# Optimization experiments

Measured on AMD Instinct MI355X. Metric: run time of the kernel, lower is better.

## Reference

```python
import jax, jax.numpy as jnp
import numpy as np

B, S, HID, NH = 2, 2048, 1024, 16
HD = HID // NH  # head dim = 64


def setup_inputs() -> dict:
    key = jax.random.key(0)
    ks = jax.random.split(key, 8)
    sc = 0.02
    return {
        "hidden_states": jax.random.normal(ks[0], (B, S, HID), jnp.float32),
        "hidden_states2": jax.random.normal(ks[1], (B, S, HID), jnp.float32),
        "Wq": jax.random.normal(ks[2], (HID, HID), jnp.float32) * sc,
        "bq": jnp.zeros((HID,), jnp.float32),
        "Wk": jax.random.normal(ks[3], (HID, HID), jnp.float32) * sc,
        "bk": jnp.zeros((HID,), jnp.float32),
        "Wv": jax.random.normal(ks[4], (HID, HID), jnp.float32) * sc,
        "bv": jnp.zeros((HID,), jnp.float32),
    }


def _split_heads(x):
    # [B, S, HID] -> [B, NH, S, HD]
    b, s, _ = x.shape
    return x.reshape(b, s, NH, HD).transpose(0, 2, 1, 3)


def reference(hidden_states, hidden_states2, Wq, bq, Wk, bk, Wv, bv):
    # Linear layers use torch convention: y = x @ W.T + b
    q = _split_heads(hidden_states @ Wq.T + bq)    # [B,NH,Sq,HD]
    k = _split_heads(hidden_states2 @ Wk.T + bk)   # [B,NH,Sk,HD]
    v = _split_heads(hidden_states2 @ Wv.T + bv)   # [B,NH,Sk,HD]
    scores = jnp.einsum("bhqd,bhkd->bhqk", q, k) / jnp.sqrt(jnp.float32(HD))
    probs = jax.nn.softmax(scores, axis=-1)        # dropout prob = 0 (eval)
    ctx = jnp.einsum("bhqk,bhkd->bhqd", probs, v)  # [B,NH,Sq,HD]
    ctx = ctx.transpose(0, 2, 1, 3).reshape(hidden_states.shape[0], hidden_states.shape[1], HID)
    return ctx
```

## Files before the change

### kernel.cpp

```cpp
#include <hip/hip_runtime.h>
#include <hip/hip_bf16.h>
#include <stdint.h>

#define B_   2
#define S_   2048
#define HID_ 1024
#define NH_  16
#define HD_  64

typedef __attribute__((ext_vector_type(4))) float f32x4;
typedef __attribute__((ext_vector_type(8))) short bf16x8;

__device__ inline unsigned short f2bf(float x) {
    __hip_bfloat16 h = __float2bfloat16(x);
    return reinterpret_cast<unsigned short&>(h);
}

__device__ inline void gload_lds16(const void* g, void* l) {
    __builtin_amdgcn_global_load_lds(
        (const __attribute__((address_space(1))) void*)g,
        (__attribute__((address_space(3))) void*)l, 16, 0, 0);
}

__device__ inline float fast_exp2(float x) {
    float r;
    asm("v_exp_f32 %0, %1" : "=v"(r) : "v"(x));
    return r;
}

__global__ __launch_bounds__(256) void cvt_all(
    const float* __restrict__ X1, const float* __restrict__ X2,
    const float* __restrict__ Wq, const float* __restrict__ Wk, const float* __restrict__ Wv,
    unsigned short* __restrict__ X1b, unsigned short* __restrict__ X2b,
    unsigned short* __restrict__ Wqb, unsigned short* __restrict__ Wkb,
    unsigned short* __restrict__ Wvb)
{
    const int id = blockIdx.x;
    const float* src;
    unsigned short* dst;
    int base;
    if (id < 2048)      { src = X1; dst = X1b; base = id; }
    else if (id < 4096) { src = X2; dst = X2b; base = id - 2048; }
    else if (id < 4608) { src = Wq; dst = Wqb; base = id - 4096; }
    else if (id < 5120) { src = Wk; dst = Wkb; base = id - 4608; }
    else                { src = Wv; dst = Wvb; base = id - 5120; }
    const size_t off = (size_t)base * 2048 + (size_t)threadIdx.x * 8;
    float4 a = *(const float4*)&src[off];
    float4 b = *(const float4*)&src[off + 4];
    unsigned short o[8] = {f2bf(a.x), f2bf(a.y), f2bf(a.z), f2bf(a.w),
                           f2bf(b.x), f2bf(b.y), f2bf(b.z), f2bf(b.w)};
    *(uint4*)&dst[off] = *(uint4*)o;
}

__global__ __launch_bounds__(256, 3) void qkv_gemm(
    const unsigned short* __restrict__ X1b, const unsigned short* __restrict__ X2b,
    const unsigned short* __restrict__ Wqb, const unsigned short* __restrict__ Wkb,
    const unsigned short* __restrict__ Wvb,
    const float* __restrict__ bq, const float* __restrict__ bk, const float* __restrict__ bv,
    unsigned short* __restrict__ Qo, unsigned short* __restrict__ Ko, unsigned short* __restrict__ Vo)
{
    const int z = blockIdx.z;
    const unsigned short* X = (z == 0) ? X1b : X2b;
    const unsigned short* W = (z == 0) ? Wqb : (z == 1 ? Wkb : Wvb);
    const float* bias = (z == 0) ? bq : (z == 1 ? bk : bv);
    unsigned short* out = (z == 0) ? Qo : (z == 1 ? Ko : Vo);

    __shared__ __align__(16) unsigned short SM[128 * 132];
    unsigned short* As = SM;
    unsigned short* Bs = SM + 128 * 64;

    const int m0 = blockIdx.x * 128;
    const int n0 = blockIdx.y * 128;
    const int t = threadIdx.x;
    const int lane = t & 63;
    const int w = t >> 6;
    const int lo = lane & 15, hi = lane >> 4;
    const int wm = w >> 1, wn = w & 1;

    const int srow = lane >> 3;
    const int scol = ((lane & 7) ^ srow) * 8;

    f32x4 acc[4][4];
    const f32x4 fzero = {0.f, 0.f, 0.f, 0.f};
    #pragma unroll
    for (int i = 0; i < 4; ++i)
        #pragma unroll
        for (int j = 0; j < 4; ++j) acc[i][j] = fzero;

    for (int kt = 0; kt < 16; ++kt) {
        __syncthreads();
        #pragma unroll
        for (int i = 0; i < 4; ++i) {
            const int r = w * 32 + i * 8 + srow;
            gload_lds16(&X[(size_t)(m0 + r) * HID_ + kt * 64 + scol],
                        &As[w * 2048 + i * 512]);
            gload_lds16(&W[(size_t)(n0 + r) * HID_ + kt * 64 + scol],
                        &Bs[w * 2048 + i * 512]);
        }
        __syncthreads();

        #pragma unroll
        for (int s = 0; s < 2; ++s) {
            const int rcol = ((s * 4 + hi) ^ (lo & 7)) * 8;
            bf16x8 a[4], b[4];
            #pragma unroll
            for (int i = 0; i < 4; ++i) {
                a[i] = *(const bf16x8*)&As[(wm * 64 + i * 16 + lo) * 64 + rcol];
                b[i] = *(const bf16x8*)&Bs[(wn * 64 + i * 16 + lo) * 64 + rcol];
            }
            #pragma unroll
            for (int i = 0; i < 4; ++i)
                #pragma unroll
                for (int j = 0; j < 4; ++j)
                    acc[i][j] = __builtin_amdgcn_mfma_f32_16x16x32_bf16(a[i], b[j], acc[i][j], 0, 0, 0);
        }
    }

    if (z != 2) {
        const float sc = (z == 0) ? 0.18033688011112042f : 1.0f;
        #pragma unroll
        for (int i = 0; i < 4; ++i) {
            #pragma unroll
            for (int j = 0; j < 4; ++j) {
                int col = n0 + wn * 64 + j * 16 + lo;
                float bb = bias[col];
                #pragma unroll
                for (int r = 0; r < 4; ++r) {
                    int row = m0 + wm * 64 + i * 16 + hi * 4 + r;
                    out[(size_t)row * HID_ + col] = f2bf((acc[i][j][r] + bb) * sc);
                }
            }
        }
    } else {
        __syncthreads();
        unsigned short* Ts = SM;
        #pragma unroll
        for (int i = 0; i < 4; ++i) {
            #pragma unroll
            for (int j = 0; j < 4; ++j) {
                int nl = wn * 64 + j * 16 + lo;
                float bb = bias[n0 + nl];
                int ml = wm * 64 + i * 16 + hi * 4;
                ushort4 pk;
                pk.x = f2bf(acc[i][j][0] + bb);
                pk.y = f2bf(acc[i][j][1] + bb);
                pk.z = f2bf(acc[i][j][2] + bb);
                pk.w = f2bf(acc[i][j][3] + bb);
                *(ushort4*)&Ts[nl * 132 + ml] = pk;
            }
        }
        __syncthreads();
        const int nn = t >> 1;
        const int mh = (t & 1) * 64;
        const int bI = m0 >> 11;
        const int sb = (m0 & 2047) + mh;
        size_t obase = (size_t)bI * ((size_t)HID_ * S_) + (size_t)(n0 + nn) * S_ + sb;
        #pragma unroll
        for (int kk = 0; kk < 8; ++kk)
            *(uint4*)&out[obase + kk * 8] = *(const uint4*)&Ts[nn * 132 + mh + kk * 8];
    }
}

__global__ __launch_bounds__(256, 2) void attn_fwd(
    const unsigned short* __restrict__ Q, const unsigned short* __restrict__ K,
    const unsigned short* __restrict__ Vt, float* __restrict__ out)
{
    __shared__ __align__(16) unsigned short Ks[2][128 * 64];
    __shared__ __align__(16) unsigned short Vs[2][64 * 128];

    const int t = threadIdx.x;
    const int lane = t & 63;
    const int w = t >> 6;
    const int lo = lane & 15, hi = lane >> 4;

    const int id = blockIdx.x + 16 * blockIdx.y;
    const int vb = (id & 7) * 64 + (id >> 3);
    const int qt = vb & 15;
    const int bh = vb >> 4;
    const int b = bh >> 4, h = bh & 15;

    const int q0 = qt * 128;
    const size_t baseQK = (size_t)b * S_ * HID_ + (size_t)h * HD_;
    const size_t baseV  = (size_t)b * ((size_t)HID_ * S_) + (size_t)h * ((size_t)HD_ * S_);

    bf16x8 qb[2][2];
    #pragma unroll
    for (int qf = 0; qf < 2; ++qf)
        #pragma unroll
        for (int st = 0; st < 2; ++st)
            qb[qf][st] = *(const bf16x8*)&Q[baseQK + (size_t)(q0 + w * 32 + qf * 16 + lo) * HID_
                                            + st * 32 + hi * 8];

    f32x4 O[2][4];
    const f32x4 fzero = {0.f, 0.f, 0.f, 0.f};
    f32x4 lacc[2] = {fzero, fzero};
    #pragma unroll
    for (int qf = 0; qf < 2; ++qf)
        #pragma unroll
        for (int c = 0; c < 4; ++c) O[qf][c] = fzero;

    bf16x8 ones;
    #pragma unroll
    for (int j = 0; j < 4; ++j) ((unsigned*)&ones)[j] = 0x3F803F80u;

    const int srow = lane >> 3;
    const int scolK = ((lane & 7) ^ srow) * 8;

    auto STAGE = [&](int buf, int kn) {
        #pragma unroll
        for (int i = 0; i < 4; ++i) {
            const int rr = w * 32 + i * 8 + srow;
            gload_lds16(&K[baseQK + (size_t)(kn + rr) * HID_ + scolK],
                        &Ks[buf][(w * 32 + i * 8) * 64]);
        }
        #pragma unroll
        for (int i = 0; i < 4; ++i) {
            const int rv = w * 16 + i * 4 + (lane >> 4);
            const int sv = ((lane & 15) ^ (rv & 15)) * 8;
            gload_lds16(&Vt[baseV + (size_t)rv * S_ + kn + sv],
                        &Vs[buf][(w * 16 + i * 4) * 128]);
        }
    };

    STAGE(0, 0);

    for (int tt = 0; tt < 16; ++tt) {
        const int cur = tt & 1;
        const bool pre = (tt < 15);

        __builtin_amdgcn_s_barrier();
        if (pre) STAGE(cur ^ 1, (tt + 1) * 128);

        if (pre) asm volatile("s_waitcnt vmcnt(8)" ::: "memory");
        else     asm volatile("s_waitcnt vmcnt(0)" ::: "memory");
        __builtin_amdgcn_s_barrier();
        __builtin_amdgcn_sched_barrier(0);

        const unsigned short* Kc = Ks[cur];
        const unsigned short* Vc = Vs[cur];

        f32x4 s[2][8];
        __builtin_amdgcn_s_setprio(1);
        #pragma unroll
        for (int n = 0; n < 8; ++n) {
            const int rc0 = (hi ^ (lo & 7)) * 8;
            const int rc1 = ((4 + hi) ^ (lo & 7)) * 8;
            bf16x8 ka0 = *(const bf16x8*)&Kc[(n * 16 + lo) * 64 + rc0];
            bf16x8 ka1 = *(const bf16x8*)&Kc[(n * 16 + lo) * 64 + rc1];
            #pragma unroll
            for (int qf = 0; qf < 2; ++qf) {
                f32x4 zc = fzero;
                zc = __builtin_amdgcn_mfma_f32_16x16x32_bf16(ka0, qb[qf][0], zc, 0, 0, 0);
                s[qf][n] = __builtin_amdgcn_mfma_f32_16x16x32_bf16(ka1, qb[qf][1], zc, 0, 0, 0);
            }
        }
        __builtin_amdgcn_s_setprio(0);

        bf16x8 pa[2][4];
        #pragma unroll
        for (int qf = 0; qf < 2; ++qf) {
            #pragma unroll
            for (int n = 0; n < 8; ++n)
                #pragma unroll
                for (int r = 0; r < 4; ++r) s[qf][n][r] = fast_exp2(s[qf][n][r]);

            #pragma unroll
            for (int st = 0; st < 4; ++st) {
                unsigned pw[4];
                #pragma unroll
                for (int p = 0; p < 2; ++p) {
                    unsigned X, Y;
                    asm("v_cvt_pk_bf16_f32 %0, %1, %2"
                        : "=v"(X) : "v"(s[qf][2 * st][2 * p]), "v"(s[qf][2 * st][2 * p + 1]));
                    asm("v_cvt_pk_bf16_f32 %0, %1, %2"
                        : "=v"(Y) : "v"(s[qf][2 * st + 1][2 * p]), "v"(s[qf][2 * st + 1][2 * p + 1]));
                    asm volatile("v_permlane32_swap_b32 %0, %1" : "+v"(X), "+v"(Y));
                    asm volatile("v_permlane16_swap_b32 %0, %1" : "+v"(X), "+v"(Y));
                    pw[p] = X;
                    pw[p + 2] = Y;
                }
                #pragma unroll
                for (int j = 0; j < 4; ++j)
                    ((unsigned*)&pa[qf][st])[j] = pw[j];
            }
        }

        __builtin_amdgcn_s_setprio(1);
        #pragma unroll
        for (int c = 0; c < 4; ++c) {
            #pragma unroll
            for (int st = 0; st < 4; ++st) {
                const int slot = ((st * 4 + hi) ^ lo) * 8;
                bf16x8 vbf = *(const bf16x8*)&Vc[(c * 16 + lo) * 128 + slot];
                #pragma unroll
                for (int qf = 0; qf < 2; ++qf)
                    O[qf][c] = __builtin_amdgcn_mfma_f32_16x16x32_bf16(pa[qf][st], vbf, O[qf][c], 0, 0, 0);
            }
        }
        #pragma unroll
        for (int qf = 0; qf < 2; ++qf)
            #pragma unroll
            for (int st = 0; st < 4; ++st)
                lacc[qf] = __builtin_amdgcn_mfma_f32_16x16x32_bf16(pa[qf][st], ones, lacc[qf], 0, 0, 0);
        __builtin_amdgcn_s_setprio(0);
    }

    #pragma unroll
    for (int qf = 0; qf < 2; ++qf) {
        float linv[4];
        #pragma unroll
        for (int r = 0; r < 4; ++r) linv[r] = 1.0f / lacc[qf][r];
        #pragma unroll
        for (int c = 0; c < 4; ++c) {
            #pragma unroll
            for (int r = 0; r < 4; ++r) {
                int q = q0 + w * 32 + qf * 16 + hi * 4 + r;
                out[(size_t)b * S_ * HID_ + (size_t)q * HID_ + h * HD_ + c * 16 + lo] =
                    O[qf][c][r] * linv[r];
            }
        }
    }
}

extern "C" void kernel_launch(void* const* d_in, const int* in_sizes, int n_in,
                              void* d_out, int out_size, void* d_ws, size_t ws_size,
                              hipStream_t stream) {
    const float* hs1 = (const float*)d_in[0];
    const float* hs2 = (const float*)d_in[1];
    const float* Wq  = (const float*)d_in[2];
    const float* bq  = (const float*)d_in[3];
    const float* Wk  = (const float*)d_in[4];
    const float* bk  = (const float*)d_in[5];
    const float* Wv  = (const float*)d_in[6];
    const float* bv  = (const float*)d_in[7];
    float* out = (float*)d_out;

    const size_t XY = (size_t)B_ * S_ * HID_;
    const size_t WW = (size_t)HID_ * HID_;
    unsigned short* Qb  = (unsigned short*)d_ws;
    unsigned short* Kb  = Qb + XY;
    unsigned short* Vb  = Kb + XY;
    unsigned short* X1b = Vb + XY;
    unsigned short* X2b = X1b + XY;
    unsigned short* Wqb = X2b + XY;
    unsigned short* Wkb = Wqb + WW;
    unsigned short* Wvb = Wkb + WW;

    cvt_all<<<5632, 256, 0, stream>>>(hs1, hs2, Wq, Wk, Wv, X1b, X2b, Wqb, Wkb, Wvb);
    qkv_gemm<<<dim3(32, 8, 3), 256, 0, stream>>>(X1b, X2b, Wqb, Wkb, Wvb,
                                                 bq, bk, bv, Qb, Kb, Vb);
    attn_fwd<<<dim3(16, 32), 256, 0, stream>>>(Qb, Kb, Vb, out);
}
```

Measured before the change: 85.26 us.

## Split attention KV tile across wave pairs with LDS reduction of partial outputs

Reassigns the four waves from each owning 32 query rows over the full 128-key tile to a 2x2 split: each wave handles 64 query rows and half the key tile. Each K/V fragment read from LDS is reused across four query fragments instead of two, which cuts LDS read traffic per MFMA. The two key-half waves combine their partial O and row sums through shared memory at the end. This costs extra barriers, an LDS reduction, larger accumulators and more register pressure.

Measured after the change: 82.39 us. 3.4% less time.

```diff
diff --git a/kernel.cpp b/kernel.cpp
--- a/kernel.cpp
+++ b/kernel.cpp
@@ -165,12 +165,14 @@
     const unsigned short* __restrict__ Q, const unsigned short* __restrict__ K,
     const unsigned short* __restrict__ Vt, float* __restrict__ out)
 {
-    __shared__ __align__(16) unsigned short Ks[2][128 * 64];
-    __shared__ __align__(16) unsigned short Vs[2][64 * 128];
+    __shared__ __align__(16) unsigned short SM2[32768];
+    unsigned short* KsBase = SM2;
+    unsigned short* VsBase = SM2 + 16384;
 
     const int t = threadIdx.x;
     const int lane = t & 63;
     const int w = t >> 6;
+    const int wq = w & 1, wk = w >> 1;
     const int lo = lane & 15, hi = lane >> 4;
 
     const int id = blockIdx.x + 16 * blockIdx.y;
@@ -183,19 +185,19 @@
     const size_t baseQK = (size_t)b * S_ * HID_ + (size_t)h * HD_;
     const size_t baseV  = (size_t)b * ((size_t)HID_ * S_) + (size_t)h * ((size_t)HD_ * S_);
 
-    bf16x8 qb[2][2];
+    bf16x8 qb[4][2];
     #pragma unroll
-    for (int qf = 0; qf < 2; ++qf)
-        #pragma unroll
-        for (int st = 0; st < 2; ++st)
-            qb[qf][st] = *(const bf16x8*)&Q[baseQK + (size_t)(q0 + w * 32 + qf * 16 + lo) * HID_
-                                            + st * 32 + hi * 8];
-
-    f32x4 O[2][4];
+    for (int qf = 0; qf < 4; ++qf)
+        #pragma unroll
+        for (int sd = 0; sd < 2; ++sd)
+            qb[qf][sd] = *(const bf16x8*)&Q[baseQK + (size_t)(q0 + wq * 64 + qf * 16 + lo) * HID_
+                                            + sd * 32 + hi * 8];
+
+    f32x4 O[4][4];
     const f32x4 fzero = {0.f, 0.f, 0.f, 0.f};
-    f32x4 lacc[2] = {fzero, fzero};
+    f32x4 lacc[4] = {fzero, fzero, fzero, fzero};
     #pragma unroll
-    for (int qf = 0; qf < 2; ++qf)
+    for (int qf = 0; qf < 4; ++qf)
         #pragma unroll
         for (int c = 0; c < 4; ++c) O[qf][c] = fzero;
 
@@ -207,18 +209,20 @@
     const int scolK = ((lane & 7) ^ srow) * 8;
 
     auto STAGE = [&](int buf, int kn) {
+        unsigned short* Kb = KsBase + buf * 8192;
+        unsigned short* Vb = VsBase + buf * 8192;
         #pragma unroll
         for (int i = 0; i < 4; ++i) {
             const int rr = w * 32 + i * 8 + srow;
             gload_lds16(&K[baseQK + (size_t)(kn + rr) * HID_ + scolK],
-                        &Ks[buf][(w * 32 + i * 8) * 64]);
+                        &Kb[(w * 32 + i * 8) * 64]);
         }
         #pragma unroll
         for (int i = 0; i < 4; ++i) {
             const int rv = w * 16 + i * 4 + (lane >> 4);
             const int sv = ((lane & 15) ^ (rv & 15)) * 8;
             gload_lds16(&Vt[baseV + (size_t)rv * S_ + kn + sv],
-                        &Vs[buf][(w * 16 + i * 4) * 128]);
+                        &Vb[(w * 16 + i * 4) * 128]);
         }
     };
 
@@ -236,87 +240,102 @@
         __builtin_amdgcn_s_barrier();
         __builtin_amdgcn_sched_barrier(0);
 
-        const unsigned short* Kc = Ks[cur];
-        const unsigned short* Vc = Vs[cur];
-
-        f32x4 s[2][8];
-        __builtin_amdgcn_s_setprio(1);
-        #pragma unroll
-        for (int n = 0; n < 8; ++n) {
-            const int rc0 = (hi ^ (lo & 7)) * 8;
-            const int rc1 = ((4 + hi) ^ (lo & 7)) * 8;
-            bf16x8 ka0 = *(const bf16x8*)&Kc[(n * 16 + lo) * 64 + rc0];
-            bf16x8 ka1 = *(const bf16x8*)&Kc[(n * 16 + lo) * 64 + rc1];
-            #pragma unroll
-            for (int qf = 0; qf < 2; ++qf) {
-                f32x4 zc = fzero;
-                zc = __builtin_amdgcn_mfma_f32_16x16x32_bf16(ka0, qb[qf][0], zc, 0, 0, 0);
-                s[qf][n] = __builtin_amdgcn_mfma_f32_16x16x32_bf16(ka1, qb[qf][1], zc, 0, 0, 0);
-            }
-        }
-        __builtin_amdgcn_s_setprio(0);
-
-        bf16x8 pa[2][4];
-        #pragma unroll
-        for (int qf = 0; qf < 2; ++qf) {
-            #pragma unroll
-            for (int n = 0; n < 8; ++n)
-                #pragma unroll
-                for (int r = 0; r < 4; ++r) s[qf][n][r] = fast_exp2(s[qf][n][r]);
-
-            #pragma unroll
-            for (int st = 0; st < 4; ++st) {
+        const unsigned short* Kc = KsBase + cur * 8192;
+        const unsigned short* Vc = VsBase + cur * 8192;
+
+        #pragma unroll
+        for (int st = 0; st < 2; ++st) {
+            f32x4 s[4][2];
+            __builtin_amdgcn_s_setprio(1);
+            #pragma unroll
+            for (int n2 = 0; n2 < 2; ++n2) {
+                const int row = wk * 64 + st * 32 + n2 * 16 + lo;
+                const int rc0 = (hi ^ (lo & 7)) * 8;
+                const int rc1 = ((4 + hi) ^ (lo & 7)) * 8;
+                bf16x8 ka0 = *(const bf16x8*)&Kc[row * 64 + rc0];
+                bf16x8 ka1 = *(const bf16x8*)&Kc[row * 64 + rc1];
+                #pragma unroll
+                for (int qf = 0; qf < 4; ++qf) {
+                    f32x4 zc = fzero;
+                    zc = __builtin_amdgcn_mfma_f32_16x16x32_bf16(ka0, qb[qf][0], zc, 0, 0, 0);
+                    s[qf][n2] = __builtin_amdgcn_mfma_f32_16x16x32_bf16(ka1, qb[qf][1], zc, 0, 0, 0);
+                }
+            }
+            __builtin_amdgcn_s_setprio(0);
+
+            bf16x8 pa[4];
+            #pragma unroll
+            for (int qf = 0; qf < 4; ++qf) {
+                #pragma unroll
+                for (int n2 = 0; n2 < 2; ++n2)
+                    #pragma unroll
+                    for (int r = 0; r < 4; ++r) s[qf][n2][r] = fast_exp2(s[qf][n2][r]);
                 unsigned pw[4];
                 #pragma unroll
                 for (int p = 0; p < 2; ++p) {
                     unsigned X, Y;
                     asm("v_cvt_pk_bf16_f32 %0, %1, %2"
-                        : "=v"(X) : "v"(s[qf][2 * st][2 * p]), "v"(s[qf][2 * st][2 * p + 1]));
+                        : "=v"(X) : "v"(s[qf][0][2 * p]), "v"(s[qf][0][2 * p + 1]));
                     asm("v_cvt_pk_bf16_f32 %0, %1, %2"
-                        : "=v"(Y) : "v"(s[qf][2 * st + 1][2 * p]), "v"(s[qf][2 * st + 1][2 * p + 1]));
+                        : "=v"(Y) : "v"(s[qf][1][2 * p]), "v"(s[qf][1][2 * p + 1]));
                     asm volatile("v_permlane32_swap_b32 %0, %1" : "+v"(X), "+v"(Y));
                     asm volatile("v_permlane16_swap_b32 %0, %1" : "+v"(X), "+v"(Y));
                     pw[p] = X;
                     pw[p + 2] = Y;
                 }
                 #pragma unroll
-                for (int j = 0; j < 4; ++j)
-                    ((unsigned*)&pa[qf][st])[j] = pw[j];
-            }
-        }
-
-        __builtin_amdgcn_s_setprio(1);
-        #pragma unroll
-        for (int c = 0; c < 4; ++c) {
-            #pragma unroll
-            for (int st = 0; st < 4; ++st) {
-                const int slot = ((st * 4 + hi) ^ lo) * 8;
+                for (int j = 0; j < 4; ++j) ((unsigned*)&pa[qf])[j] = pw[j];
+            }
+
+            __builtin_amdgcn_s_setprio(1);
+            #pragma unroll
+            for (int c = 0; c < 4; ++c) {
+                const int slot = ((wk * 8 + st * 4 + hi) ^ lo) * 8;
                 bf16x8 vbf = *(const bf16x8*)&Vc[(c * 16 + lo) * 128 + slot];
                 #pragma unroll
-                for (int qf = 0; qf < 2; ++qf)
-                    O[qf][c] = __builtin_amdgcn_mfma_f32_16x16x32_bf16(pa[qf][st], vbf, O[qf][c], 0, 0, 0);
-            }
-        }
-        #pragma unroll
-        for (int qf = 0; qf < 2; ++qf)
-            #pragma unroll
-            for (int st = 0; st < 4; ++st)
-                lacc[qf] = __builtin_amdgcn_mfma_f32_16x16x32_bf16(pa[qf][st], ones, lacc[qf], 0, 0, 0);
-        __builtin_amdgcn_s_setprio(0);
-    }
-
-    #pragma unroll
-    for (int qf = 0; qf < 2; ++qf) {
-        float linv[4];
-        #pragma unroll
-        for (int r = 0; r < 4; ++r) linv[r] = 1.0f / lacc[qf][r];
-        #pragma unroll
-        for (int c = 0; c < 4; ++c) {
-            #pragma unroll
-            for (int r = 0; r < 4; ++r) {
-                int q = q0 + w * 32 + qf * 16 + hi * 4 + r;
-                out[(size_t)b * S_ * HID_ + (size_t)q * HID_ + h * HD_ + c * 16 + lo] =
-                    O[qf][c][r] * linv[r];
+                for (int qf = 0; qf < 4; ++qf)
+                    O[qf][c] = __builtin_amdgcn_mfma_f32_16x16x32_bf16(pa[qf], vbf, O[qf][c], 0, 0, 0);
+            }
+            #pragma unroll
+            for (int qf = 0; qf < 4; ++qf)
+                lacc[qf] = __builtin_amdgcn_mfma_f32_16x16x32_bf16(pa[qf], ones, lacc[qf], 0, 0, 0);
+            __builtin_amdgcn_s_setprio(0);
+        }
+    }
+
+    __syncthreads();
+    float* Obuf = (float*)SM2;
+    float* Lbuf = (float*)(SM2 + 16896);
+
+    if (wk == 1) {
+        #pragma unroll
+        for (int qf = 0; qf < 4; ++qf) {
+            #pragma unroll
+            for (int c = 0; c < 4; ++c)
+                *(float4*)&Obuf[(c * 16 + lo) * 132 + wq * 64 + qf * 16 + hi * 4] =
+                    *(float4*)&O[qf][c];
+            #pragma unroll
+            for (int r = 0; r < 4; ++r)
+                Lbuf[wq * 64 + qf * 16 + hi * 4 + r] = lacc[qf][r];
+        }
+    }
+    __syncthreads();
+    if (wk == 0) {
+        #pragma unroll
+        for (int qf = 0; qf < 4; ++qf) {
+            float linv[4];
+            #pragma unroll
+            for (int r = 0; r < 4; ++r)
+                linv[r] = 1.0f / (lacc[qf][r] + Lbuf[wq * 64 + qf * 16 + hi * 4 + r]);
+            #pragma unroll
+            for (int c = 0; c < 4; ++c) {
+                float4 p = *(float4*)&Obuf[(c * 16 + lo) * 132 + wq * 64 + qf * 16 + hi * 4];
+                #pragma unroll
+                for (int r = 0; r < 4; ++r) {
+                    int q = q0 + wq * 64 + qf * 16 + hi * 4 + r;
+                    out[(size_t)b * S_ * HID_ + (size_t)q * HID_ + h * HD_ + c * 16 + lo] =
+                        (O[qf][c][r] + (&p.x)[r]) * linv[r];
+                }
             }
         }
     }
```
